# Performance work log

Hardware: AMD Instinct MI355X
Metric: run time of the kernel (lower is better)

The kernel has to match this reference:

```python
import jax, jax.numpy as jnp
import numpy as np

B, P, L1, L2, LOUT, F = 20000, 1, 16, 16, 49, 512


def setup_inputs() -> dict:
    key = jax.random.key(0)
    k1, k2, k3 = jax.random.split(key, 3)
    x1 = jax.random.normal(k1, (B, P, L1, F), dtype=jnp.float32)
    x2 = jax.random.normal(k2, (B, P, L2, F), dtype=jnp.float32)
    # Clebsch-Gordan coefficient tensor [(l1max+1)^2, (l2max+1)^2, (lout+1)^2].
    # Random stand-in; the module treats it as a dense constant tensor.
    cg = jax.random.normal(k3, (L1, L2, LOUT), dtype=jnp.float32)
    return {"x1": x1, "x2": x2, "cg": cg}


def reference(x1, x2, cg):
    # Non-pseudotensor branch of TensorProduct.forward:
    # output[:, 0:1, :, :] = einsum('...lf, ...mf, lmn -> ...nf', x1, x2, cg)
    # b: batch, p: parity (size 1), l/m: input sph-harm dims, n: output sph-harm dim, f: channels
    out = jnp.einsum('bplf,bpmf,lmn->bpnf', x1, x2, cg)
    return out
```

## Files before the change

kernel.cpp:

```cpp
#include <hip/hip_runtime.h>
#include <hip/hip_bf16.h>


#define TP_L    16
#define TP_K    256
#define TP_NOUT 49
#define TP_NPAD 64
#define TP_F    512

typedef short short8 __attribute__((ext_vector_type(8)));
typedef float f32x4  __attribute__((ext_vector_type(4)));

static __device__ __forceinline__ short f2bf(float f) {
    unsigned u = __float_as_uint(f);
    u += 0x7fffu + ((u >> 16) & 1u);
    return (short)(u >> 16);
}

__global__ void prep_cg_kernel(const float* __restrict__ cg, short* __restrict__ cgT) {
    int idx = blockIdx.x * 256 + threadIdx.x;
    int n = idx >> 8;
    int k = idx & 255;
    float v = (n < TP_NOUT) ? cg[k * TP_NOUT + n] : 0.0f;
    cgT[idx] = f2bf(v);
}

__global__ void __launch_bounds__(512, 4) tp_kernel(
    const float* __restrict__ x1, const float* __restrict__ x2,
    const short* __restrict__ cgT, float* __restrict__ out)
{
    __shared__ float4 s1v[TP_L * TP_F / 4];
    __shared__ float4 s2v[TP_L * TP_F / 4];

    const int b   = blockIdx.x;
    const int tid = threadIdx.x;

    const float4* g1 = (const float4*)(x1 + (size_t)b * (TP_L * TP_F));
    const float4* g2 = (const float4*)(x2 + (size_t)b * (TP_L * TP_F));
#pragma unroll
    for (int i = 0; i < 4; ++i) {
        s1v[tid + i * 512] = g1[tid + i * 512];
        s2v[tid + i * 512] = g2[tid + i * 512];
    }
    __syncthreads();

    const float* sx1 = (const float*)s1v;
    const float* sx2 = (const float*)s2v;

    const int lane = tid & 63;
    const int w    = tid >> 6;
    const int fl   = lane & 15;
    const int g    = lane >> 4;
    const int hg   = g >> 1;
    const int qg   = g & 1;
    const int fb   = w * 64;

    f32x4 acc[4][4];
#pragma unroll
    for (int nt = 0; nt < 4; ++nt)
#pragma unroll
        for (int ft = 0; ft < 4; ++ft)
            acc[nt][ft] = (f32x4){0.f, 0.f, 0.f, 0.f};

#pragma unroll
    for (int s = 0; s < 8; ++s) {
        short8 a[4];
#pragma unroll
        for (int nt = 0; nt < 4; ++nt) {
            a[nt] = *(const short8*)(cgT + (nt * 16 + fl) * TP_K + s * 32 + g * 8);
        }
#pragma unroll
        for (int ft = 0; ft < 4; ++ft) {
            const int f = fb + ft * 16 + fl;
            const float x1v = sx1[(2 * s + hg) * TP_F + f];
            const float* x2c = &sx2[(qg * 8) * TP_F + f];
            short8 bfr;
#pragma unroll
            for (int i = 0; i < 8; ++i) {
                bfr[i] = f2bf(x1v * x2c[i * TP_F]);
            }
#pragma unroll
            for (int nt = 0; nt < 4; ++nt) {
                acc[nt][ft] = __builtin_amdgcn_mfma_f32_16x16x32_bf16(
                    a[nt], bfr, acc[nt][ft], 0, 0, 0);
            }
        }
    }

    float* outb = out + (size_t)b * (TP_NOUT * TP_F);
#pragma unroll
    for (int nt = 0; nt < 4; ++nt) {
#pragma unroll
        for (int j = 0; j < 4; ++j) {
            const int n = nt * 16 + g * 4 + j;
            if (n < TP_NOUT) {
#pragma unroll
                for (int ft = 0; ft < 4; ++ft) {
                    outb[n * TP_F + fb + ft * 16 + fl] = acc[nt][ft][j];
                }
            }
        }
    }
}

extern "C" void kernel_launch(void* const* d_in, const int* in_sizes, int n_in,
                              void* d_out, int out_size, void* d_ws, size_t ws_size,
                              hipStream_t stream) {
    const float* x1 = (const float*)d_in[0];
    const float* x2 = (const float*)d_in[1];
    const float* cg = (const float*)d_in[2];
    float* out = (float*)d_out;
    short* cgT = (short*)d_ws;

    const int B = in_sizes[0] / (TP_L * TP_F);

    prep_cg_kernel<<<TP_NPAD, 256, 0, stream>>>(cg, cgT);
    tp_kernel<<<B, 512, 0, stream>>>(x1, x2, cgT, out);
}
```

Baseline: 2.406 ms.

## Split batch rows across two blocks and stage output through LDS for vector stores

After: 3.748 ms. 55.8% more time.

```diff
diff --git a/kernel.cpp b/kernel.cpp
--- a/kernel.cpp
+++ b/kernel.cpp
@@ -3,10 +3,9 @@
 
 
 #define TP_L    16
-#define TP_K    256
 #define TP_NOUT 49
-#define TP_NPAD 64
 #define TP_F    512
+#define HF      256
 
 typedef short short8 __attribute__((ext_vector_type(8)));
 typedef float f32x4  __attribute__((ext_vector_type(4)));
@@ -25,27 +24,31 @@
     cgT[idx] = f2bf(v);
 }
 
-__global__ void __launch_bounds__(512, 4) tp_kernel(
+__global__ void __launch_bounds__(512, 6) tp_kernel(
     const float* __restrict__ x1, const float* __restrict__ x2,
     const short* __restrict__ cgT, float* __restrict__ out)
 {
-    __shared__ float4 s1v[TP_L * TP_F / 4];
-    __shared__ float4 s2v[TP_L * TP_F / 4];
+    __shared__ float smem[8192];
 
-    const int b   = blockIdx.x;
-    const int tid = threadIdx.x;
+    const int bid  = blockIdx.x;
+    const int b    = bid >> 1;
+    const int half = bid & 1;
+    const int tid  = threadIdx.x;
 
-    const float4* g1 = (const float4*)(x1 + (size_t)b * (TP_L * TP_F));
-    const float4* g2 = (const float4*)(x2 + (size_t)b * (TP_L * TP_F));
+    const float* x1b = x1 + (size_t)b * (TP_L * TP_F) + half * HF;
+    const float* x2b = x2 + (size_t)b * (TP_L * TP_F) + half * HF;
+
 #pragma unroll
-    for (int i = 0; i < 4; ++i) {
-        s1v[tid + i * 512] = g1[tid + i * 512];
-        s2v[tid + i * 512] = g2[tid + i * 512];
+    for (int i = 0; i < 2; ++i) {
+        const int idx = tid + i * 512;
+        const int row = idx >> 6, c4 = idx & 63;
+        ((f32x4*)smem)[idx]        = *(const f32x4*)(x1b + row * TP_F + c4 * 4);
+        ((f32x4*)smem)[1024 + idx] = *(const f32x4*)(x2b + row * TP_F + c4 * 4);
     }
     __syncthreads();
 
-    const float* sx1 = (const float*)s1v;
-    const float* sx2 = (const float*)s2v;
+    const float* sx1 = smem;
+    const float* sx2 = smem + 4096;
 
     const int lane = tid & 63;
     const int w    = tid >> 6;
@@ -53,52 +56,74 @@
     const int g    = lane >> 4;
     const int hg   = g >> 1;
     const int qg   = g & 1;
-    const int fb   = w * 64;
+    const int wf   = w * 32;
 
-    f32x4 acc[4][4];
+    f32x4 acc[4][2];
 #pragma unroll
     for (int nt = 0; nt < 4; ++nt)
 #pragma unroll
-        for (int ft = 0; ft < 4; ++ft)
+        for (int ft = 0; ft < 2; ++ft)
             acc[nt][ft] = (f32x4){0.f, 0.f, 0.f, 0.f};
 
 #pragma unroll
     for (int s = 0; s < 8; ++s) {
         short8 a[4];
 #pragma unroll
-        for (int nt = 0; nt < 4; ++nt) {
-            a[nt] = *(const short8*)(cgT + (nt * 16 + fl) * TP_K + s * 32 + g * 8);
-        }
+        for (int nt = 0; nt < 4; ++nt)
+            a[nt] = *(const short8*)(cgT + (nt * 16 + fl) * 256 + s * 32 + g * 8);
 #pragma unroll
-        for (int ft = 0; ft < 4; ++ft) {
-            const int f = fb + ft * 16 + fl;
-            const float x1v = sx1[(2 * s + hg) * TP_F + f];
-            const float* x2c = &sx2[(qg * 8) * TP_F + f];
+        for (int ft = 0; ft < 2; ++ft) {
+            const int f = wf + ft * 16 + fl;
+            const float x1v = sx1[(2 * s + hg) * HF + f];
+            const float* x2c = &sx2[(qg * 8) * HF + f];
             short8 bfr;
 #pragma unroll
-            for (int i = 0; i < 8; ++i) {
-                bfr[i] = f2bf(x1v * x2c[i * TP_F]);
-            }
+            for (int i = 0; i < 8; ++i)
+                bfr[i] = f2bf(x1v * x2c[i * HF]);
 #pragma unroll
-            for (int nt = 0; nt < 4; ++nt) {
+            for (int nt = 0; nt < 4; ++nt)
                 acc[nt][ft] = __builtin_amdgcn_mfma_f32_16x16x32_bf16(
                     a[nt], bfr, acc[nt][ft], 0, 0, 0);
-            }
         }
     }
 
-    float* outb = out + (size_t)b * (TP_NOUT * TP_F);
+    float* outb = out + (size_t)b * (TP_NOUT * TP_F) + half * HF;
+
+    __syncthreads();
+
 #pragma unroll
-    for (int nt = 0; nt < 4; ++nt) {
+    for (int nt = 0; nt < 2; ++nt)
 #pragma unroll
-        for (int j = 0; j < 4; ++j) {
-            const int n = nt * 16 + g * 4 + j;
-            if (n < TP_NOUT) {
+        for (int j = 0; j < 4; ++j)
 #pragma unroll
-                for (int ft = 0; ft < 4; ++ft) {
-                    outb[n * TP_F + fb + ft * 16 + fl] = acc[nt][ft][j];
-                }
-            }
+            for (int ft = 0; ft < 2; ++ft)
+                smem[(nt * 16 + g * 4 + j) * HF + wf + ft * 16 + fl] = acc[nt][ft][j];
+    __syncthreads();
+#pragma unroll
+    for (int it = 0; it < 4; ++it) {
+        const int idx = it * 512 + tid;
+        const int row = idx >> 6, c4 = idx & 63;
+        *(f32x4*)(outb + (size_t)row * TP_F + c4 * 4) = ((const f32x4*)smem)[idx];
+    }
+    __syncthreads();
+
+#pragma unroll
+    for (int j = 0; j < 4; ++j)
+#pragma unroll
+        for (int ft = 0; ft < 2; ++ft)
+            smem[(g * 4 + j) * HF + wf + ft * 16 + fl] = acc[2][ft][j];
+    if (g == 0) {
+#pragma unroll
+        for (int ft = 0; ft < 2; ++ft)
+            smem[16 * HF + wf + ft * 16 + fl] = acc[3][ft][0];
+    }
+    __syncthreads();
+#pragma unroll
+    for (int it = 0; it < 3; ++it) {
+        const int idx = it * 512 + tid;
+        if (idx < 17 * 64) {
+            const int row = idx >> 6, c4 = idx & 63;
+            *(f32x4*)(outb + (size_t)(32 + row) * TP_F + c4 * 4) = ((const f32x4*)smem)[idx];
         }
     }
 }
@@ -114,6 +139,6 @@
 
     const int B = in_sizes[0] / (TP_L * TP_F);
 
-    prep_cg_kernel<<<TP_NPAD, 256, 0, stream>>>(cg, cgT);
-    tp_kernel<<<B, 512, 0, stream>>>(x1, x2, cgT, out);
+    prep_cg_kernel<<<64, 256, 0, stream>>>(cg, cgT);
+    tp_kernel<<<2 * B, 512, 0, stream>>>(x1, x2, cgT, out);
 }
```
